# Kernel tuning notes

Hardware: AMD Instinct MI355X
Metric: run time of the kernel (lower is better)

The kernel has to match this reference:

```python
import jax, jax.numpy as jnp
import numpy as np

N_HEAD = 16
HEAD_DIM = 64

def setup_inputs() -> dict:
    key = jax.random.key(0)
    k1, k2, k3 = jax.random.split(key, 3)
    B, S, D = 4, 2048, 1024
    x = jax.random.normal(k1, (B, S, D), dtype=jnp.float32)
    mask = jnp.tril(jnp.ones((S, S), dtype=bool))[None, None]  # (1,1,S,S) causal
    w_attn = jax.random.normal(k2, (D, 3 * D), dtype=jnp.float32) * (1.0 / np.sqrt(D))
    b_attn = jnp.zeros((3 * D,), dtype=jnp.float32)
    w_proj = jax.random.normal(k3, (D, D), dtype=jnp.float32) * (1.0 / np.sqrt(D))
    b_proj = jnp.zeros((D,), dtype=jnp.float32)
    return {"x": x, "mask": mask, "w_attn": w_attn, "b_attn": b_attn,
            "w_proj": w_proj, "b_proj": b_proj}

def reference(x, mask, w_attn, b_attn, w_proj, b_proj):
    B, S, D = x.shape
    H, hd = N_HEAD, HEAD_DIM
    qkv = x @ w_attn + b_attn                      # (B,S,3D)
    q, k, v = jnp.split(qkv, 3, axis=-1)
    q = q.reshape(B, S, H, hd).transpose(0, 2, 1, 3)  # (B,H,S,hd)
    k = k.reshape(B, S, H, hd).transpose(0, 2, 1, 3)
    v = v.reshape(B, S, H, hd).transpose(0, 2, 1, 3)
    scores = jnp.einsum('bhqd,bhkd->bhqk', q, k) / jnp.sqrt(jnp.float32(hd))
    scores = jnp.where(mask, scores, jnp.float32(-1e10))
    weights = jax.nn.softmax(scores, axis=-1)      # dropout is identity (deterministic=True)
    attn = jnp.einsum('bhqk,bhkd->bhqd', weights, v)
    attn = attn.transpose(0, 2, 1, 3).reshape(B, S, D)
    return attn @ w_proj + b_proj
```

## Files before the change

### kernel.cpp

```cpp
#include <hip/hip_runtime.h>
#include <hip/hip_bf16.h>
#include <stdint.h>


typedef uint16_t u16;
typedef __bf16 bf16x8 __attribute__((ext_vector_type(8)));
typedef __bf16 bf16x4 __attribute__((ext_vector_type(4)));
typedef short s16x4 __attribute__((ext_vector_type(4)));
typedef float f32x4 __attribute__((ext_vector_type(4)));

#define S_LEN 2048
#define DMODEL 1024
#define NHEAD 16
#define HDIM 64
#define MTOT 8192
#define NQKV 3072

__device__ __forceinline__ u16 f2bf(float f) {
    union { float f; uint32_t u; } v; v.f = f;
    uint32_t u = v.u;
    return (u16)((u + 0x7fffu + ((u >> 16) & 1u)) >> 16);
}

__device__ __forceinline__ s16x4 bits4(bf16x4 v) {
    union { bf16x4 b; s16x4 s; } u; u.b = v; return u.s;
}

__device__ __forceinline__ f32x4 mfma16(bf16x4 a, bf16x4 b, f32x4 c) {
    return __builtin_amdgcn_mfma_f32_16x16x16bf16_1k(bits4(a), bits4(b), c, 0, 0, 0);
}

__device__ __forceinline__ void async_load16(const void* g, void* l) {
    __builtin_amdgcn_global_load_lds(
        (__attribute__((address_space(1))) void*)g,
        (__attribute__((address_space(3))) void*)l,
        16, 0, 0);
}

#define NCONV (MTOT * DMODEL / 4 / 256)
#define NWAT  ((NQKV / 64) * (DMODEL / 64))
#define NWPT  ((DMODEL / 64) * (DMODEL / 64))

__device__ __forceinline__ void transpose_tile(
    const float* __restrict__ in, u16* __restrict__ out, int R, int C,
    int bx, int by, int tid)
{
    __shared__ float tile[64][65];
    int r0 = by * 64, c0 = bx * 64;
    #pragma unroll
    for (int i = 0; i < 16; ++i) {
        int idx = tid + i * 256;
        int r = idx >> 6, c = idx & 63;
        tile[r][c] = in[(size_t)(r0 + r) * C + c0 + c];
    }
    __syncthreads();
    #pragma unroll
    for (int i = 0; i < 16; ++i) {
        int idx = tid + i * 256;
        int c = idx >> 6, r = idx & 63;
        out[(size_t)(c0 + c) * R + r0 + r] = f2bf(tile[r][c]);
    }
}

__global__ void prep_kernel(
    const float4* __restrict__ x4, ushort4* __restrict__ xb4,
    const float* __restrict__ w_attn, u16* __restrict__ wat,
    const float* __restrict__ w_proj, u16* __restrict__ wpt)
{
    const int bid = blockIdx.x;
    const int tid = threadIdx.x;
    if (bid < NCONV) {
        int i = bid * 256 + tid;
        float4 f = x4[i];
        ushort4 o;
        o.x = f2bf(f.x); o.y = f2bf(f.y); o.z = f2bf(f.z); o.w = f2bf(f.w);
        xb4[i] = o;
    } else if (bid < NCONV + NWAT) {
        int b2 = bid - NCONV;
        transpose_tile(w_attn, wat, DMODEL, NQKV, b2 % (NQKV / 64), b2 / (NQKV / 64), tid);
    } else {
        int b3 = bid - NCONV - NWAT;
        transpose_tile(w_proj, wpt, DMODEL, DMODEL, b3 % (DMODEL / 64), b3 / (DMODEL / 64), tid);
    }
}

__global__ void transpose_v_kernel(const u16* __restrict__ qkv, u16* __restrict__ vt) {
    __shared__ u16 tile[64 * 66];
    const int tid = threadIdx.x;
    const int stile = blockIdx.x, bh = blockIdx.y;
    const int b = bh >> 4, h = bh & 15;
    const u16* src = qkv + ((size_t)b * S_LEN + stile * 64) * NQKV + 2 * DMODEL + h * HDIM;
    #pragma unroll
    for (int it = 0; it < 2; ++it) {
        int item = it * 256 + tid;
        int s = item >> 3, d0 = (item & 7) * 8;
        bf16x8 v = *(const bf16x8*)(src + (size_t)s * NQKV + d0);
        const u16* vu = (const u16*)&v;
        #pragma unroll
        for (int j = 0; j < 8; ++j) tile[(d0 + j) * 66 + s] = vu[j];
    }
    __syncthreads();
    #pragma unroll
    for (int it = 0; it < 2; ++it) {
        int item = it * 256 + tid;
        int d = item >> 3, s0 = (item & 7) * 8;
        union { u16 u[8]; uint4 v; } pk;
        #pragma unroll
        for (int j = 0; j < 8; ++j) pk.u[j] = tile[d * 66 + s0 + j];
        *(uint4*)(vt + ((size_t)bh * 64 + d) * S_LEN + stile * 64 + s0) = pk.v;
    }
}

template<int NF, bool OUT_BF16>
__global__ __launch_bounds__(512, 2) void gemm16q(
    const u16* __restrict__ A, const u16* __restrict__ Bt,
    const float* __restrict__ bias, void* __restrict__ C,
    int M, int N, int K)
{
    constexpr int NBH = NF / 2;
    constexpr int BSLOT = NF * 4096;
    __shared__ __attribute__((aligned(16))) u16 sm[32768 + 2 * BSLOT];
    u16* const As = sm;
    u16* const Bs = sm + 32768;

    const int tid = threadIdx.x;
    const int wave = tid >> 6, lane = tid & 63;
    const int l15 = lane & 15, q4 = lane >> 4;
    const int wm = wave >> 2, wn = wave & 3;

    const int bid = (int)blockIdx.x;
    const int xcd = bid & 7;
    const int lx  = bid >> 3;
    const int MB  = M >> 8;
    const int PM  = MB >> 3;
    const int nb  = lx / PM;
    const int mb  = xcd * PM + (lx - nb * PM);
    const int m0 = mb << 8, n0 = nb * NF * 64;

    const u16* Ag = A + (size_t)m0 * K;
    const u16* Bg = Bt + (size_t)n0 * K;

    const int srow = tid >> 3;
    const size_t goff0 = (size_t)srow * K + (size_t)(((tid & 7) ^ (srow & 7)) * 8);
    const size_t goff1 = goff0 + (size_t)64 * K;
    const int ldso = tid * 8;

    const int ck0 = (q4 ^ (l15 & 7)) * 8;
    const int ck1 = ((4 + q4) ^ (l15 & 7)) * 8;
    const int rb0 = (wn * NF * 16 + l15) * 64;

    f32x4 acc[8][NF] = {};
    const int T = K >> 6;

#define STAGE_A(t_, h_) do { \
    const u16* ga_ = Ag + (size_t)(h_) * 128 * K + (size_t)(t_) * 64; \
    u16* da_ = As + (((t_) & 1) * 2 + (h_)) * 8192; \
    async_load16(ga_ + goff0, da_ + ldso); \
    async_load16(ga_ + goff1, da_ + ldso + 4096); \
} while (0)

#define STAGE_B(t_, h_) do { \
    const u16* gb_ = Bg + (size_t)(h_) * 128 * K + (size_t)(t_) * 64; \
    u16* db_ = Bs + ((t_) & 1) * BSLOT + (h_) * 8192; \
    async_load16(gb_ + goff0, db_ + ldso); \
    async_load16(gb_ + goff1, db_ + ldso + 4096); \
} while (0)

#define LOAD_AF(P_) do { \
    af[0][0] = *(const bf16x8*)(Ah + ((2 * (P_)) * 16 + l15) * 64 + ck0); \
    af[0][1] = *(const bf16x8*)(Ah + ((2 * (P_)) * 16 + l15) * 64 + ck1); \
    af[1][0] = *(const bf16x8*)(Ah + ((2 * (P_) + 1) * 16 + l15) * 64 + ck0); \
    af[1][1] = *(const bf16x8*)(Ah + ((2 * (P_) + 1) * 16 + l15) * 64 + ck1); \
} while (0)

#define PHASE_MFMA(P_) do { \
    __builtin_amdgcn_s_barrier(); \
    __builtin_amdgcn_s_setprio(1); \
    _Pragma("unroll") \
    for (int i_ = 0; i_ < 2; ++i_) \
        _Pragma("unroll") \
        for (int nf_ = 0; nf_ < NF; ++nf_) \
            _Pragma("unroll") \
            for (int kk_ = 0; kk_ < 2; ++kk_) \
                acc[2 * (P_) + i_][nf_] = __builtin_amdgcn_mfma_f32_16x16x32_bf16( \
                    af[i_][kk_], bfr[nf_][kk_], acc[2 * (P_) + i_][nf_], 0, 0, 0); \
    __builtin_amdgcn_s_setprio(0); \
} while (0)

    STAGE_A(0, 0); STAGE_A(0, 1);
    STAGE_B(0, 0); if constexpr (NBH == 2) STAGE_B(0, 1);
    if (T > 1) {
        STAGE_B(1, 0); if constexpr (NBH == 2) STAGE_B(1, 1);
        if constexpr (NBH == 2) asm volatile("s_waitcnt vmcnt(4)");
        else                    asm volatile("s_waitcnt vmcnt(2)");
    } else {
        asm volatile("s_waitcnt vmcnt(0)");
    }
    __builtin_amdgcn_sched_barrier(0);
    __builtin_amdgcn_s_barrier();

    for (int t = 0; t < T; ++t) {
        const int par = t & 1;
        const u16* Ah = As + (par * 2 + wm) * 8192;
        const u16* Bl = Bs + par * BSLOT;

        bf16x8 af[2][2], bfr[NF][2];

        #pragma unroll
        for (int nf = 0; nf < NF; ++nf) {
            bfr[nf][0] = *(const bf16x8*)(Bl + rb0 + nf * (16 * 64) + ck0);
            bfr[nf][1] = *(const bf16x8*)(Bl + rb0 + nf * (16 * 64) + ck1);
        }
        LOAD_AF(0);
        if (t + 1 < T) STAGE_A(t + 1, 0);
        PHASE_MFMA(0);
        __builtin_amdgcn_s_barrier();

        LOAD_AF(1);
        if (t + 1 < T) STAGE_A(t + 1, 1);
        PHASE_MFMA(1);
        __builtin_amdgcn_s_barrier();

        LOAD_AF(2);
        if (t + 2 < T) STAGE_B(t + 2, 0);
        PHASE_MFMA(2);
        __builtin_amdgcn_s_barrier();

        LOAD_AF(3);
        if constexpr (NBH == 2) { if (t + 2 < T) STAGE_B(t + 2, 1); }
        PHASE_MFMA(3);
        if (t + 1 < T) {
            if (t + 2 < T) {
                if constexpr (NBH == 2) asm volatile("s_waitcnt vmcnt(4)");
                else                    asm volatile("s_waitcnt vmcnt(2)");
            } else {
                asm volatile("s_waitcnt vmcnt(0)");
            }
            __builtin_amdgcn_sched_barrier(0);
            __builtin_amdgcn_s_barrier();
        }
    }

#undef STAGE_A
#undef STAGE_B
#undef LOAD_AF
#undef PHASE_MFMA

    #pragma unroll
    for (int mf = 0; mf < 8; ++mf) {
        const int row = m0 + wm * 128 + mf * 16 + q4 * 4;
        #pragma unroll
        for (int nf = 0; nf < NF; ++nf) {
            const int col = n0 + wn * NF * 16 + nf * 16 + l15;
            const float bv = bias[col];
            #pragma unroll
            for (int r = 0; r < 4; ++r) {
                float v = acc[mf][nf][r] + bv;
                if (OUT_BF16) ((u16*)C)[(size_t)(row + r) * N + col] = f2bf(v);
                else          ((float*)C)[(size_t)(row + r) * N + col] = v;
            }
        }
    }
}

__device__ __forceinline__ void stage_tiles(
    const u16* __restrict__ qkv, const u16* __restrict__ vt,
    size_t base, int bh, int h, int w, int srow8, int schunk,
    int kt, u16* __restrict__ KsB, u16* __restrict__ VsB)
{
    #pragma unroll
    for (int q = 0; q < 2; ++q) {
        int rloc = w * 16 + q * 8 + srow8;
        int sc = ((schunk ^ (rloc & 7)) * 8);
        async_load16(qkv + (base + (size_t)kt * 64 + rloc) * (size_t)NQKV + DMODEL + h * HDIM + sc,
                     KsB + (w * 16 + q * 8) * 64);
        async_load16(vt + ((size_t)bh * 64 + rloc) * S_LEN + kt * 64 + sc,
                     VsB + (w * 16 + q * 8) * 64);
    }
}

__device__ __forceinline__ void attn_pass(
    int qt, const u16* __restrict__ qkv, const u16* __restrict__ vt,
    __bf16* __restrict__ outb, u16 (*Ks)[64 * 64], u16 (*Vs)[64 * 64],
    int w, int lane, int bh, int h, size_t base)
{
    const int l15 = lane & 15, q4 = lane >> 4;
    const int srow8 = lane >> 3, schunk = lane & 7;

    const float QSCALE = 0.125f * 1.44269504f;
    bf16x8 qf[2][2];
    #pragma unroll
    for (int mh = 0; mh < 2; ++mh) {
        int qrow = qt * 128 + mh * 64 + w * 16 + l15;
        #pragma unroll
        for (int kc = 0; kc < 2; ++kc) {
            bf16x8 raw = *(const bf16x8*)(qkv + (base + qrow) * (size_t)NQKV + h * HDIM + kc * 32 + q4 * 8);
            bf16x8 sc;
            #pragma unroll
            for (int j = 0; j < 8; ++j) sc[j] = (__bf16)((float)raw[j] * QSCALE);
            qf[mh][kc] = sc;
        }
    }

    bf16x4 ones4;
    #pragma unroll
    for (int j = 0; j < 4; ++j) ones4[j] = (__bf16)1.0f;

    f32x4 o0[4] = {}, o1[4] = {};
    f32x4 la0 = {}, la1 = {};

    const int ktlast = 2 * qt + 1;

    __syncthreads();
    stage_tiles(qkv, vt, base, bh, h, w, srow8, schunk, 0, Ks[0], Vs[0]);
    if (ktlast >= 1)
        stage_tiles(qkv, vt, base, bh, h, w, srow8, schunk, 1, Ks[1], Vs[1]);

    for (int kt = 0; kt <= 2 * qt; ++kt) {
        const int buf = kt % 3;
        __syncthreads();
        int pf = kt + 2;
        if (pf <= ktlast)
            stage_tiles(qkv, vt, base, bh, h, w, srow8, schunk, pf, Ks[pf % 3], Vs[pf % 3]);

        f32x4 st0[4] = {}, st1[4] = {};
        #pragma unroll
        for (int nt = 0; nt < 4; ++nt) {
            int n = nt * 16 + l15;
            #pragma unroll
            for (int kc = 0; kc < 2; ++kc) {
                int ch = (((kc * 4 + q4) ^ (n & 7)) * 8);
                bf16x8 kf = *(const bf16x8*)(&Ks[buf][n * 64 + ch]);
                st0[nt] = __builtin_amdgcn_mfma_f32_16x16x32_bf16(kf, qf[0][kc], st0[nt], 0, 0, 0);
                st1[nt] = __builtin_amdgcn_mfma_f32_16x16x32_bf16(kf, qf[1][kc], st1[nt], 0, 0, 0);
            }
        }

        if (kt == 2 * qt) {
            #pragma unroll
            for (int nt = 0; nt < 4; ++nt)
                #pragma unroll
                for (int r = 0; r < 4; ++r) {
                    int keyl = nt * 16 + q4 * 4 + r;
                    if (keyl > w * 16 + l15) st0[nt][r] = -1e30f;
                }
        }

        bf16x4 pb0[4], pb1[4];
        #pragma unroll
        for (int nt = 0; nt < 4; ++nt)
            #pragma unroll
            for (int r = 0; r < 4; ++r) {
                pb0[nt][r] = (__bf16)__builtin_amdgcn_exp2f(st0[nt][r]);
                pb1[nt][r] = (__bf16)__builtin_amdgcn_exp2f(st1[nt][r]);
            }

        #pragma unroll
        for (int nt = 0; nt < 4; ++nt) {
            #pragma unroll
            for (int mt = 0; mt < 4; ++mt) {
                int row = mt * 16 + l15;
                int ch = (nt * 2 + (q4 >> 1)) ^ (row & 7);
                bf16x4 vf = *(const bf16x4*)(&Vs[buf][row * 64 + ch * 8 + (q4 & 1) * 4]);
                o0[mt] = mfma16(vf, pb0[nt], o0[mt]);
                o1[mt] = mfma16(vf, pb1[nt], o1[mt]);
            }
            la0 = mfma16(ones4, pb0[nt], la0);
            la1 = mfma16(ones4, pb1[nt], la1);
        }
    }

    {
        const int buf = ktlast % 3;
        __syncthreads();

        f32x4 st1[4] = {};
        #pragma unroll
        for (int nt = 0; nt < 4; ++nt) {
            int n = nt * 16 + l15;
            #pragma unroll
            for (int kc = 0; kc < 2; ++kc) {
                int ch = (((kc * 4 + q4) ^ (n & 7)) * 8);
                bf16x8 kf = *(const bf16x8*)(&Ks[buf][n * 64 + ch]);
                st1[nt] = __builtin_amdgcn_mfma_f32_16x16x32_bf16(kf, qf[1][kc], st1[nt], 0, 0, 0);
            }
        }
        bf16x4 pb1[4];
        #pragma unroll
        for (int nt = 0; nt < 4; ++nt)
            #pragma unroll
            for (int r = 0; r < 4; ++r) {
                int keyl = nt * 16 + q4 * 4 + r;
                float s = (keyl > w * 16 + l15) ? -1e30f : st1[nt][r];
                pb1[nt][r] = (__bf16)__builtin_amdgcn_exp2f(s);
            }
        #pragma unroll
        for (int nt = 0; nt < 4; ++nt) {
            #pragma unroll
            for (int mt = 0; mt < 4; ++mt) {
                int row = mt * 16 + l15;
                int ch = (nt * 2 + (q4 >> 1)) ^ (row & 7);
                bf16x4 vf = *(const bf16x4*)(&Vs[buf][row * 64 + ch * 8 + (q4 & 1) * 4]);
                o1[mt] = mfma16(vf, pb1[nt], o1[mt]);
            }
            la1 = mfma16(ones4, pb1[nt], la1);
        }
    }

    float inv0 = 1.0f / la0[0], inv1 = 1.0f / la1[0];
    int row0 = qt * 128 + w * 16 + l15;
    int row1 = row0 + 64;
    #pragma unroll
    for (int mt = 0; mt < 4; ++mt) {
        union { __bf16 b[4]; ushort4 v; } p0, p1;
        #pragma unroll
        for (int r = 0; r < 4; ++r) {
            p0.b[r] = (__bf16)(o0[mt][r] * inv0);
            p1.b[r] = (__bf16)(o1[mt][r] * inv1);
        }
        int col = h * HDIM + mt * 16 + q4 * 4;
        *(ushort4*)(&outb[(base + row0) * (size_t)DMODEL + col]) = p0.v;
        *(ushort4*)(&outb[(base + row1) * (size_t)DMODEL + col]) = p1.v;
    }
}

__global__ __launch_bounds__(256, 3) void attn_kernel(
    const u16* __restrict__ qkv, const u16* __restrict__ vt, u16* __restrict__ out)
{
    __shared__ __attribute__((aligned(16))) u16 Ks[3][64 * 64];
    __shared__ __attribute__((aligned(16))) u16 Vs[3][64 * 64];

    const int tid = threadIdx.x;
    const int w = tid >> 6, lane = tid & 63;
    const int bh = blockIdx.y;
    const int b = bh >> 4, h = bh & 15;
    const size_t base = (size_t)b * S_LEN;
    const int NT = (int)gridDim.x * 2;

    attn_pass(NT - 1 - (int)blockIdx.x, qkv, vt, (__bf16*)out, Ks, Vs, w, lane, bh, h, base);
    attn_pass((int)blockIdx.x,          qkv, vt, (__bf16*)out, Ks, Vs, w, lane, bh, h, base);
}

extern "C" void kernel_launch(void* const* d_in, const int* in_sizes, int n_in,
                              void* d_out, int out_size, void* d_ws, size_t ws_size,
                              hipStream_t stream) {
    const float* x      = (const float*)d_in[0];
    const float* w_attn = (const float*)d_in[2];
    const float* b_attn = (const float*)d_in[3];
    const float* w_proj = (const float*)d_in[4];
    const float* b_proj = (const float*)d_in[5];

    u16* xb   = (u16*)d_ws;
    u16* wat  = xb  + (size_t)MTOT * DMODEL;
    u16* wpt  = wat + (size_t)NQKV * DMODEL;
    u16* qkv  = wpt + (size_t)DMODEL * DMODEL;
    u16* attn = qkv + (size_t)MTOT * NQKV;
    u16* vt   = xb;

    prep_kernel<<<NCONV + NWAT + NWPT, 256, 0, stream>>>(
        (const float4*)x, (ushort4*)xb, w_attn, wat, w_proj, wpt);

    gemm16q<4, true><<<dim3((MTOT / 256) * (NQKV / 256)), 512, 0, stream>>>(
        xb, wat, b_attn, (void*)qkv, MTOT, NQKV, DMODEL);

    transpose_v_kernel<<<dim3(S_LEN / 64, 4 * NHEAD), 256, 0, stream>>>(qkv, vt);

    attn_kernel<<<dim3(S_LEN / 256, 4 * NHEAD), 256, 0, stream>>>(qkv, vt, attn);

    gemm16q<2, false><<<dim3((MTOT / 256) * (DMODEL / 128)), 512, 0, stream>>>(
        attn, wpt, b_proj, d_out, MTOT, DMODEL, DMODEL);
}
```

Measured before the change: 268.9 us.

## Fuse V transpose into QKV GEMM epilogue and widen GEMM phases

```diff
diff --git a/kernel.cpp b/kernel.cpp
--- a/kernel.cpp
+++ b/kernel.cpp
@@ -15,6 +15,7 @@
 #define HDIM 64
 #define MTOT 8192
 #define NQKV 3072
+#define QKN 2048
 
 __device__ __forceinline__ u16 f2bf(float f) {
     union { float f; uint32_t u; } v; v.f = f;
@@ -84,38 +85,11 @@
     }
 }
 
-__global__ void transpose_v_kernel(const u16* __restrict__ qkv, u16* __restrict__ vt) {
-    __shared__ u16 tile[64 * 66];
-    const int tid = threadIdx.x;
-    const int stile = blockIdx.x, bh = blockIdx.y;
-    const int b = bh >> 4, h = bh & 15;
-    const u16* src = qkv + ((size_t)b * S_LEN + stile * 64) * NQKV + 2 * DMODEL + h * HDIM;
-    #pragma unroll
-    for (int it = 0; it < 2; ++it) {
-        int item = it * 256 + tid;
-        int s = item >> 3, d0 = (item & 7) * 8;
-        bf16x8 v = *(const bf16x8*)(src + (size_t)s * NQKV + d0);
-        const u16* vu = (const u16*)&v;
-        #pragma unroll
-        for (int j = 0; j < 8; ++j) tile[(d0 + j) * 66 + s] = vu[j];
-    }
-    __syncthreads();
-    #pragma unroll
-    for (int it = 0; it < 2; ++it) {
-        int item = it * 256 + tid;
-        int d = item >> 3, s0 = (item & 7) * 8;
-        union { u16 u[8]; uint4 v; } pk;
-        #pragma unroll
-        for (int j = 0; j < 8; ++j) pk.u[j] = tile[d * 66 + s0 + j];
-        *(uint4*)(vt + ((size_t)bh * 64 + d) * S_LEN + stile * 64 + s0) = pk.v;
-    }
-}
-
-template<int NF, bool OUT_BF16>
-__global__ __launch_bounds__(512, 2) void gemm16q(
+template<int NF, int OUTMODE>
+__global__ __launch_bounds__(512, 2) void gemm16q2(
     const u16* __restrict__ A, const u16* __restrict__ Bt,
     const float* __restrict__ bias, void* __restrict__ C,
-    int M, int N, int K)
+    u16* __restrict__ vt, int M, int N, int K)
 {
     constexpr int NBH = NF / 2;
     constexpr int BSLOT = NF * 4096;
@@ -166,24 +140,25 @@
     async_load16(gb_ + goff1, db_ + ldso + 4096); \
 } while (0)
 
-#define LOAD_AF(P_) do { \
-    af[0][0] = *(const bf16x8*)(Ah + ((2 * (P_)) * 16 + l15) * 64 + ck0); \
-    af[0][1] = *(const bf16x8*)(Ah + ((2 * (P_)) * 16 + l15) * 64 + ck1); \
-    af[1][0] = *(const bf16x8*)(Ah + ((2 * (P_) + 1) * 16 + l15) * 64 + ck0); \
-    af[1][1] = *(const bf16x8*)(Ah + ((2 * (P_) + 1) * 16 + l15) * 64 + ck1); \
+#define LOAD_AF4(P_) do { \
+    _Pragma("unroll") \
+    for (int i_ = 0; i_ < 4; ++i_) { \
+        af[i_][0] = *(const bf16x8*)(Ah + ((4 * (P_) + i_) * 16 + l15) * 64 + ck0); \
+        af[i_][1] = *(const bf16x8*)(Ah + ((4 * (P_) + i_) * 16 + l15) * 64 + ck1); \
+    } \
 } while (0)
 
-#define PHASE_MFMA(P_) do { \
+#define PHASE_MFMA4(P_) do { \
     __builtin_amdgcn_s_barrier(); \
     __builtin_amdgcn_s_setprio(1); \
     _Pragma("unroll") \
-    for (int i_ = 0; i_ < 2; ++i_) \
+    for (int i_ = 0; i_ < 4; ++i_) \
         _Pragma("unroll") \
         for (int nf_ = 0; nf_ < NF; ++nf_) \
             _Pragma("unroll") \
             for (int kk_ = 0; kk_ < 2; ++kk_) \
-                acc[2 * (P_) + i_][nf_] = __builtin_amdgcn_mfma_f32_16x16x32_bf16( \
-                    af[i_][kk_], bfr[nf_][kk_], acc[2 * (P_) + i_][nf_], 0, 0, 0); \
+                acc[4 * (P_) + i_][nf_] = __builtin_amdgcn_mfma_f32_16x16x32_bf16( \
+                    af[i_][kk_], bfr[nf_][kk_], acc[4 * (P_) + i_][nf_], 0, 0, 0); \
     __builtin_amdgcn_s_setprio(0); \
 } while (0)
 
@@ -204,31 +179,21 @@
         const u16* Ah = As + (par * 2 + wm) * 8192;
         const u16* Bl = Bs + par * BSLOT;
 
-        bf16x8 af[2][2], bfr[NF][2];
+        bf16x8 af[4][2], bfr[NF][2];
 
         #pragma unroll
         for (int nf = 0; nf < NF; ++nf) {
             bfr[nf][0] = *(const bf16x8*)(Bl + rb0 + nf * (16 * 64) + ck0);
             bfr[nf][1] = *(const bf16x8*)(Bl + rb0 + nf * (16 * 64) + ck1);
         }
-        LOAD_AF(0);
-        if (t + 1 < T) STAGE_A(t + 1, 0);
-        PHASE_MFMA(0);
+        LOAD_AF4(0);
+        if (t + 1 < T) { STAGE_A(t + 1, 0); STAGE_A(t + 1, 1); }
+        PHASE_MFMA4(0);
         __builtin_amdgcn_s_barrier();
 
-        LOAD_AF(1);
-        if (t + 1 < T) STAGE_A(t + 1, 1);
-        PHASE_MFMA(1);
-        __builtin_amdgcn_s_barrier();
-
-        LOAD_AF(2);
-        if (t + 2 < T) STAGE_B(t + 2, 0);
-        PHASE_MFMA(2);
-        __builtin_amdgcn_s_barrier();
-
-        LOAD_AF(3);
-        if constexpr (NBH == 2) { if (t + 2 < T) STAGE_B(t + 2, 1); }
-        PHASE_MFMA(3);
+        LOAD_AF4(1);
+        if (t + 2 < T) { STAGE_B(t + 2, 0); if constexpr (NBH == 2) STAGE_B(t + 2, 1); }
+        PHASE_MFMA4(1);
         if (t + 1 < T) {
             if (t + 2 < T) {
                 if constexpr (NBH == 2) asm volatile("s_waitcnt vmcnt(4)");
@@ -243,28 +208,44 @@
 
 #undef STAGE_A
 #undef STAGE_B
-#undef LOAD_AF
-#undef PHASE_MFMA
+#undef LOAD_AF4
+#undef PHASE_MFMA4
 
     #pragma unroll
     for (int mf = 0; mf < 8; ++mf) {
         const int row = m0 + wm * 128 + mf * 16 + q4 * 4;
         #pragma unroll
         for (int nf = 0; nf < NF; ++nf) {
-            const int col = n0 + wn * NF * 16 + nf * 16 + l15;
+            const int col0 = n0 + wn * NF * 16 + nf * 16;
+            const int col = col0 + l15;
             const float bv = bias[col];
-            #pragma unroll
-            for (int r = 0; r < 4; ++r) {
-                float v = acc[mf][nf][r] + bv;
-                if (OUT_BF16) ((u16*)C)[(size_t)(row + r) * N + col] = f2bf(v);
-                else          ((float*)C)[(size_t)(row + r) * N + col] = v;
+            if constexpr (OUTMODE == 0) {
+                #pragma unroll
+                for (int r = 0; r < 4; ++r)
+                    ((float*)C)[(size_t)(row + r) * N + col] = acc[mf][nf][r] + bv;
+            } else {
+                if (col0 < 2 * DMODEL) {
+                    #pragma unroll
+                    for (int r = 0; r < 4; ++r)
+                        ((u16*)C)[(size_t)(row + r) * QKN + col] = f2bf(acc[mf][nf][r] + bv);
+                } else {
+                    const int vc = col - 2 * DMODEL;
+                    const int bh = (row >> 11) * NHEAD + (vc >> 6);
+                    const int dd = vc & 63;
+                    const int s  = row & (S_LEN - 1);
+                    union { __bf16 b[4]; ushort4 v; } pk;
+                    #pragma unroll
+                    for (int r = 0; r < 4; ++r)
+                        pk.b[r] = (__bf16)(acc[mf][nf][r] + bv);
+                    *(ushort4*)(&vt[((size_t)bh * 64 + dd) * S_LEN + s]) = pk.v;
+                }
             }
         }
     }
 }
 
 __device__ __forceinline__ void stage_tiles(
-    const u16* __restrict__ qkv, const u16* __restrict__ vt,
+    const u16* __restrict__ qk, const u16* __restrict__ vt,
     size_t base, int bh, int h, int w, int srow8, int schunk,
     int kt, u16* __restrict__ KsB, u16* __restrict__ VsB)
 {
@@ -272,7 +253,7 @@
     for (int q = 0; q < 2; ++q) {
         int rloc = w * 16 + q * 8 + srow8;
         int sc = ((schunk ^ (rloc & 7)) * 8);
-        async_load16(qkv + (base + (size_t)kt * 64 + rloc) * (size_t)NQKV + DMODEL + h * HDIM + sc,
+        async_load16(qk + (base + (size_t)kt * 64 + rloc) * (size_t)QKN + DMODEL + h * HDIM + sc,
                      KsB + (w * 16 + q * 8) * 64);
         async_load16(vt + ((size_t)bh * 64 + rloc) * S_LEN + kt * 64 + sc,
                      VsB + (w * 16 + q * 8) * 64);
@@ -280,7 +261,7 @@
 }
 
 __device__ __forceinline__ void attn_pass(
-    int qt, const u16* __restrict__ qkv, const u16* __restrict__ vt,
+    int qt, const u16* __restrict__ qk, const u16* __restrict__ vt,
     __bf16* __restrict__ outb, u16 (*Ks)[64 * 64], u16 (*Vs)[64 * 64],
     int w, int lane, int bh, int h, size_t base)
 {
@@ -294,7 +275,7 @@
         int qrow = qt * 128 + mh * 64 + w * 16 + l15;
         #pragma unroll
         for (int kc = 0; kc < 2; ++kc) {
-            bf16x8 raw = *(const bf16x8*)(qkv + (base + qrow) * (size_t)NQKV + h * HDIM + kc * 32 + q4 * 8);
+            bf16x8 raw = *(const bf16x8*)(qk + (base + qrow) * (size_t)QKN + h * HDIM + kc * 32 + q4 * 8);
             bf16x8 sc;
             #pragma unroll
             for (int j = 0; j < 8; ++j) sc[j] = (__bf16)((float)raw[j] * QSCALE);
@@ -312,16 +293,16 @@
     const int ktlast = 2 * qt + 1;
 
     __syncthreads();
-    stage_tiles(qkv, vt, base, bh, h, w, srow8, schunk, 0, Ks[0], Vs[0]);
+    stage_tiles(qk, vt, base, bh, h, w, srow8, schunk, 0, Ks[0], Vs[0]);
     if (ktlast >= 1)
-        stage_tiles(qkv, vt, base, bh, h, w, srow8, schunk, 1, Ks[1], Vs[1]);
+        stage_tiles(qk, vt, base, bh, h, w, srow8, schunk, 1, Ks[1], Vs[1]);
 
     for (int kt = 0; kt <= 2 * qt; ++kt) {
         const int buf = kt % 3;
         __syncthreads();
         int pf = kt + 2;
         if (pf <= ktlast)
-            stage_tiles(qkv, vt, base, bh, h, w, srow8, schunk, pf, Ks[pf % 3], Vs[pf % 3]);
+            stage_tiles(qk, vt, base, bh, h, w, srow8, schunk, pf, Ks[pf % 3], Vs[pf % 3]);
 
         f32x4 st0[4] = {}, st1[4] = {};
         #pragma unroll
@@ -425,7 +406,7 @@
 }
 
 __global__ __launch_bounds__(256, 3) void attn_kernel(
-    const u16* __restrict__ qkv, const u16* __restrict__ vt, u16* __restrict__ out)
+    const u16* __restrict__ qk, const u16* __restrict__ vt, u16* __restrict__ out)
 {
     __shared__ __attribute__((aligned(16))) u16 Ks[3][64 * 64];
     __shared__ __attribute__((aligned(16))) u16 Vs[3][64 * 64];
@@ -437,8 +418,8 @@
     const size_t base = (size_t)b * S_LEN;
     const int NT = (int)gridDim.x * 2;
 
-    attn_pass(NT - 1 - (int)blockIdx.x, qkv, vt, (__bf16*)out, Ks, Vs, w, lane, bh, h, base);
-    attn_pass((int)blockIdx.x,          qkv, vt, (__bf16*)out, Ks, Vs, w, lane, bh, h, base);
+    attn_pass(NT - 1 - (int)blockIdx.x, qk, vt, (__bf16*)out, Ks, Vs, w, lane, bh, h, base);
+    attn_pass((int)blockIdx.x,          qk, vt, (__bf16*)out, Ks, Vs, w, lane, bh, h, base);
 }
 
 extern "C" void kernel_launch(void* const* d_in, const int* in_sizes, int n_in,
@@ -453,20 +434,18 @@
     u16* xb   = (u16*)d_ws;
     u16* wat  = xb  + (size_t)MTOT * DMODEL;
     u16* wpt  = wat + (size_t)NQKV * DMODEL;
-    u16* qkv  = wpt + (size_t)DMODEL * DMODEL;
-    u16* attn = qkv + (size_t)MTOT * NQKV;
-    u16* vt   = xb;
+    u16* qk   = wpt + (size_t)DMODEL * DMODEL;
+    u16* vt   = qk  + (size_t)MTOT * QKN;
+    u16* attn = vt  + (size_t)64 * 64 * S_LEN;
 
     prep_kernel<<<NCONV + NWAT + NWPT, 256, 0, stream>>>(
         (const float4*)x, (ushort4*)xb, w_attn, wat, w_proj, wpt);
 
-    gemm16q<4, true><<<dim3((MTOT / 256) * (NQKV / 256)), 512, 0, stream>>>(
-        xb, wat, b_attn, (void*)qkv, MTOT, NQKV, DMODEL);
-
-    transpose_v_kernel<<<dim3(S_LEN / 64, 4 * NHEAD), 256, 0, stream>>>(qkv, vt);
-
-    attn_kernel<<<dim3(S_LEN / 256, 4 * NHEAD), 256, 0, stream>>>(qkv, vt, attn);
-
-    gemm16q<2, false><<<dim3((MTOT / 256) * (DMODEL / 128)), 512, 0, stream>>>(
-        attn, wpt, b_proj, d_out, MTOT, DMODEL, DMODEL);
-}
+    gemm16q2<4, 1><<<dim3((MTOT / 256) * (NQKV / 256)), 512, 0, stream>>>(
+        xb, wat, b_attn, (void*)qk, vt, MTOT, NQKV, DMODEL);
+
+    attn_kernel<<<dim3(S_LEN / 256, 4 * NHEAD), 256, 0, stream>>>(qk, vt, attn);
+
+    gemm16q2<2, 0><<<dim3((MTOT / 256) * (DMODEL / 128)), 512, 0, stream>>>(
+        attn, wpt, b_proj, d_out, nullptr, MTOT, DMODEL, DMODEL);
+}
```

After: 261.9 us. -2.6%, faster.
